# Optimization experiments

Measured on AMD Instinct MI355X. Metric: run time of the kernel, lower is better.

## Reference

```python
import jax, jax.numpy as jnp
import numpy as np

# bitsandbytes FP4 code table (magnitudes), signed -> 16 codes (two zeros, harmless)
_FP4_MAGS = np.array([0.0, 0.0052083333, 1.0/6.0, 0.25, 1.0/3.0, 0.5, 2.0/3.0, 1.0], dtype=np.float32)
_FP4_CODES = np.sort(np.concatenate([-_FP4_MAGS, _FP4_MAGS])).astype(np.float32)
_FP4_BOUNDS = ((_FP4_CODES[:-1] + _FP4_CODES[1:]) * 0.5).astype(np.float32)
_BLOCK = 64  # bnb default FP4 blocksize


def fp4_roundtrip(w):
    """Simulate bnb quantize_fp4 -> dequantize_fp4 (blockwise absmax + nearest FP4 code)."""
    shp = w.shape
    wf = w.reshape(-1, _BLOCK)                              # [n_blocks, 64]
    absmax = jnp.max(jnp.abs(wf), axis=1, keepdims=True)    # per-block scale
    n = wf / jnp.maximum(absmax, 1e-12)                     # normalized to [-1, 1]
    idx = jnp.searchsorted(jnp.asarray(_FP4_BOUNDS), n)     # nearest-code index
    deq = jnp.asarray(_FP4_CODES)[idx] * absmax             # dequantized values
    return deq.reshape(shp)


def setup_inputs() -> dict:
    key = jax.random.key(0)
    k1, k2 = jax.random.split(key)
    in_features, out_features, tokens = 4096, 11008, 8192
    x = jax.random.normal(k1, (tokens, in_features), dtype=jnp.float32)
    weight = jax.random.normal(k2, (out_features, in_features), dtype=jnp.float32) * 0.1
    bias = jnp.zeros((out_features,), dtype=jnp.float32)
    return {"x": x, "weight": weight, "bias": bias}


def reference(x, weight, bias):
    # forward path with quantized weights: dequantize FP4 then matmul + bias
    w = fp4_roundtrip(weight)                # [out, in]
    return jnp.matmul(x, w.T) + bias         # [tokens, out]
```

## Files before the change

kernel.cpp:

```cpp
#include <hip/hip_runtime.h>
#include <hip/hip_bf16.h>
#include <stdint.h>

#define M_DIM 8192
#define N_DIM 11008
#define K_DIM 4096
#define NQB 44032
#define NCB 16384

typedef __attribute__((ext_vector_type(8))) short bf16x8;
typedef __attribute__((ext_vector_type(4))) float f32x4;

__device__ const float kCodes[16] = {
    -1.0f, -(float)(2.0 / 3.0), -0.5f, -(float)(1.0 / 3.0), -0.25f,
    -(float)(1.0 / 6.0), -0.0052083333f, -0.0f,
    0.0f, 0.0052083333f, (float)(1.0 / 6.0), 0.25f,
    (float)(1.0 / 3.0), 0.5f, (float)(2.0 / 3.0), 1.0f};

__device__ __forceinline__ float fp4_bound(int i) {
  return (kCodes[i] + kCodes[i + 1]) * 0.5f;
}

__device__ __forceinline__ unsigned short f2bf(float f) {
  uint32_t u = __float_as_uint(f);
  u = (u + 0x7FFFu + ((u >> 16) & 1u)) >> 16;
  return (unsigned short)u;
}

__device__ __forceinline__ float fp4_rt(float w, float d, float am) {
  float n = w / d;
  int idx = 0;
#pragma unroll
  for (int i = 0; i < 15; ++i) idx += (n > fp4_bound(i)) ? 1 : 0;
  return kCodes[idx] * am;
}

__device__ __forceinline__ uint32_t pack2(float lo, float hi) {
  return (uint32_t)f2bf(lo) | ((uint32_t)f2bf(hi) << 16);
}

__global__ void prep_kernel(const float* __restrict__ W,
                            unsigned short* __restrict__ Wq,
                            const float* __restrict__ X,
                            uint32_t* __restrict__ Y) {
  const int bid = blockIdx.x;
  if (bid < NQB) {
    int t = bid * 256 + threadIdx.x;
    size_t base = (size_t)t * 4;
    float4 v = *reinterpret_cast<const float4*>(W + base);
    float am =
        fmaxf(fmaxf(fabsf(v.x), fabsf(v.y)), fmaxf(fabsf(v.z), fabsf(v.w)));
    am = fmaxf(am, __shfl_xor(am, 1));
    am = fmaxf(am, __shfl_xor(am, 2));
    am = fmaxf(am, __shfl_xor(am, 4));
    am = fmaxf(am, __shfl_xor(am, 8));
    float d = fmaxf(am, 1e-12f);
    ushort4 o;
    o.x = f2bf(fp4_rt(v.x, d, am));
    o.y = f2bf(fp4_rt(v.y, d, am));
    o.z = f2bf(fp4_rt(v.z, d, am));
    o.w = f2bf(fp4_rt(v.w, d, am));
    *reinterpret_cast<ushort4*>(Wq + base) = o;
  } else {
    int t = (bid - NQB) * 256 + threadIdx.x;
    size_t base = (size_t)t * 8;
    float4 a = *reinterpret_cast<const float4*>(X + base);
    float4 b = *reinterpret_cast<const float4*>(X + base + 4);
    uint4 o;
    o.x = pack2(a.x, a.y);
    o.y = pack2(a.z, a.w);
    o.z = pack2(b.x, b.y);
    o.w = pack2(b.z, b.w);
    *reinterpret_cast<uint4*>(Y + (size_t)t * 4) = o;
  }
}

#define GLOAD(src, dst)                                                        \
  __builtin_amdgcn_global_load_lds(                                           \
      (const __attribute__((address_space(1))) void*)(src),                   \
      (__attribute__((address_space(3))) void*)(dst), 16, 0, 0)

#define WAIT_LGKM(N)                                                           \
  asm volatile("s_waitcnt lgkmcnt(" #N ")" ::: "memory");                      \
  __builtin_amdgcn_sched_barrier(0);                                           \
  __builtin_amdgcn_s_setprio(1);

#define ENDBAR()                                                               \
  __builtin_amdgcn_s_setprio(0);                                               \
  __builtin_amdgcn_sched_barrier(0);                                           \
  __builtin_amdgcn_s_barrier();

#define ENDBAR_VM0()                                                           \
  __builtin_amdgcn_s_setprio(0);                                               \
  __builtin_amdgcn_sched_barrier(0);                                           \
  asm volatile("s_waitcnt vmcnt(0)" ::: "memory");                             \
  __builtin_amdgcn_s_barrier();

__global__ __launch_bounds__(512, 2) void gemm256_kernel(
    const short* __restrict__ A, const short* __restrict__ B,
    const float* __restrict__ bias, float* __restrict__ C) {
  __shared__ short lds[2][4][8192];

  const int tid = threadIdx.x;
  const int wave = tid >> 6;
  const int lane = tid & 63;
  const int l15 = lane & 15;
  const int q4 = lane >> 4;
  const int wm = wave >> 2;
  const int wn = wave & 3;

  const int bid = blockIdx.x;
  const int g = bid & 7;
  const int idx = bid >> 3;
  const int brow = (g * 4 + (idx & 3)) * 256;
  const int bcol = (idx >> 2) * 256;

  const int srow = tid >> 3;
  const int scol = ((tid & 7) ^ ((tid >> 3) & 7)) << 3;
  const short* Asrc = A + (size_t)(brow + srow) * K_DIM + scol;
  const short* Bsrc = B + (size_t)(bcol + srow) * K_DIM + scol;
  const int wu0 = wave * 512;
  const int wu1 = 4096 + wave * 512;

  auto stageA = [&](int buf, int half, int t) {
    const short* s = Asrc + (size_t)half * 128 * K_DIM + t * 64;
    GLOAD(s, &lds[buf][half][wu0]);
    GLOAD(s + (size_t)64 * K_DIM, &lds[buf][half][wu1]);
  };
  auto stageB = [&](int buf, int half, int t) {
    const short* s = Bsrc + (size_t)half * 128 * K_DIM + t * 64;
    GLOAD(s, &lds[buf][2 + half][wu0]);
    GLOAD(s + (size_t)64 * K_DIM, &lds[buf][2 + half][wu1]);
  };

  const int offk0 = ((q4 ^ (l15 & 7)) << 4);
  const int offk1 = offk0 ^ 64;
  const char* aP[2] = {(const char*)&lds[0][wm][0] + l15 * 128,
                       (const char*)&lds[1][wm][0] + l15 * 128};
  const char* bP[2] = {
      (const char*)&lds[0][2 + (wn >> 1)][0] + (wn & 1) * 8192 + l15 * 128,
      (const char*)&lds[1][2 + (wn >> 1)][0] + (wn & 1) * 8192 + l15 * 128};

  f32x4 acc[8][4] = {};
  bf16x8 afA[4], afB[4], bfA[4], bfB[4];

  stageB(0, 0, 0);
  stageB(0, 1, 0);
  stageA(0, 0, 0);
  stageA(0, 1, 0);
  stageB(1, 0, 1);
  asm volatile("s_waitcnt vmcnt(2)" ::: "memory");
  __builtin_amdgcn_s_barrier();
#pragma unroll
  for (int m = 0; m < 4; ++m) afA[m] = *(const bf16x8*)(aP[0] + m * 2048 + offk0);
#pragma unroll
  for (int n = 0; n < 4; ++n) bfA[n] = *(const bf16x8*)(bP[0] + n * 2048 + offk0);

  for (int i = 0; i < 32; ++i) {
    const int t1 = 2 * i + 1;
    const int t2 = (2 * i + 2 < 64) ? 2 * i + 2 : 63;
    const int t3 = (2 * i + 3 < 64) ? 2 * i + 3 : 63;

#pragma unroll
    for (int m = 0; m < 4; ++m)
      afB[m] = *(const bf16x8*)(aP[0] + (4 + m) * 2048 + offk0);
    stageB(1, 1, t1);
    WAIT_LGKM(4);
#pragma unroll
    for (int m = 0; m < 4; ++m)
#pragma unroll
      for (int n = 0; n < 4; ++n)
        acc[m][n] = __builtin_amdgcn_mfma_f32_16x16x32_bf16(afA[m], bfA[n],
                                                            acc[m][n], 0, 0, 0);
    ENDBAR();

#pragma unroll
    for (int m = 0; m < 4; ++m)
      afA[m] = *(const bf16x8*)(aP[0] + m * 2048 + offk1);
#pragma unroll
    for (int n = 0; n < 4; ++n)
      bfB[n] = *(const bf16x8*)(bP[0] + n * 2048 + offk1);
    stageA(1, 0, t1);
    stageA(1, 1, t1);
    WAIT_LGKM(8);
#pragma unroll
    for (int m = 0; m < 4; ++m)
#pragma unroll
      for (int n = 0; n < 4; ++n)
        acc[4 + m][n] = __builtin_amdgcn_mfma_f32_16x16x32_bf16(
            afB[m], bfA[n], acc[4 + m][n], 0, 0, 0);
    ENDBAR();

#pragma unroll
    for (int m = 0; m < 4; ++m)
      afB[m] = *(const bf16x8*)(aP[0] + (4 + m) * 2048 + offk1);
    WAIT_LGKM(4);
#pragma unroll
    for (int m = 0; m < 4; ++m)
#pragma unroll
      for (int n = 0; n < 4; ++n)
        acc[m][n] = __builtin_amdgcn_mfma_f32_16x16x32_bf16(afA[m], bfB[n],
                                                            acc[m][n], 0, 0, 0);
    ENDBAR_VM0();

#pragma unroll
    for (int m = 0; m < 4; ++m)
      afA[m] = *(const bf16x8*)(aP[1] + m * 2048 + offk0);
#pragma unroll
    for (int n = 0; n < 4; ++n)
      bfA[n] = *(const bf16x8*)(bP[1] + n * 2048 + offk0);
    stageB(0, 0, t2);
    WAIT_LGKM(8);
#pragma unroll
    for (int m = 0; m < 4; ++m)
#pragma unroll
      for (int n = 0; n < 4; ++n)
        acc[4 + m][n] = __builtin_amdgcn_mfma_f32_16x16x32_bf16(
            afB[m], bfB[n], acc[4 + m][n], 0, 0, 0);
    ENDBAR();

#pragma unroll
    for (int m = 0; m < 4; ++m)
      afB[m] = *(const bf16x8*)(aP[1] + (4 + m) * 2048 + offk0);
    stageB(0, 1, t2);
    WAIT_LGKM(4);
#pragma unroll
    for (int m = 0; m < 4; ++m)
#pragma unroll
      for (int n = 0; n < 4; ++n)
        acc[m][n] = __builtin_amdgcn_mfma_f32_16x16x32_bf16(afA[m], bfA[n],
                                                            acc[m][n], 0, 0, 0);
    ENDBAR();

#pragma unroll
    for (int m = 0; m < 4; ++m)
      afA[m] = *(const bf16x8*)(aP[1] + m * 2048 + offk1);
#pragma unroll
    for (int n = 0; n < 4; ++n)
      bfB[n] = *(const bf16x8*)(bP[1] + n * 2048 + offk1);
    stageA(0, 0, t2);
    stageA(0, 1, t2);
    WAIT_LGKM(8);
#pragma unroll
    for (int m = 0; m < 4; ++m)
#pragma unroll
      for (int n = 0; n < 4; ++n)
        acc[4 + m][n] = __builtin_amdgcn_mfma_f32_16x16x32_bf16(
            afB[m], bfA[n], acc[4 + m][n], 0, 0, 0);
    ENDBAR();

#pragma unroll
    for (int m = 0; m < 4; ++m)
      afB[m] = *(const bf16x8*)(aP[1] + (4 + m) * 2048 + offk1);
    WAIT_LGKM(4);
#pragma unroll
    for (int m = 0; m < 4; ++m)
#pragma unroll
      for (int n = 0; n < 4; ++n)
        acc[m][n] = __builtin_amdgcn_mfma_f32_16x16x32_bf16(afA[m], bfB[n],
                                                            acc[m][n], 0, 0, 0);
    ENDBAR_VM0();

#pragma unroll
    for (int m = 0; m < 4; ++m)
      afA[m] = *(const bf16x8*)(aP[0] + m * 2048 + offk0);
#pragma unroll
    for (int n = 0; n < 4; ++n)
      bfA[n] = *(const bf16x8*)(bP[0] + n * 2048 + offk0);
    stageB(1, 0, t3);
    WAIT_LGKM(8);
#pragma unroll
    for (int m = 0; m < 4; ++m)
#pragma unroll
      for (int n = 0; n < 4; ++n)
        acc[4 + m][n] = __builtin_amdgcn_mfma_f32_16x16x32_bf16(
            afB[m], bfB[n], acc[4 + m][n], 0, 0, 0);
    ENDBAR();
  }

  const int crow0 = brow + wm * 128 + q4 * 4;
  const int ccol0 = bcol + wn * 64 + l15;
#pragma unroll
  for (int n = 0; n < 4; ++n) {
    const float bv = bias[ccol0 + n * 16];
#pragma unroll
    for (int m = 0; m < 8; ++m) {
      const size_t rb = (size_t)(crow0 + m * 16) * N_DIM + (ccol0 + n * 16);
#pragma unroll
      for (int j = 0; j < 4; ++j) C[rb + (size_t)j * N_DIM] = acc[m][n][j] + bv;
    }
  }
}

__global__ __launch_bounds__(256, 2) void gemm_bt_kernel(
    const short* __restrict__ A, const short* __restrict__ B,
    const float* __restrict__ bias, float* __restrict__ C) {
  __shared__ short Alds[128 * 32];
  __shared__ short Blds[128 * 32];

  const int tid = threadIdx.x;
  const int wave = tid >> 6;
  const int lane = tid & 63;
  const int wr = wave >> 1;
  const int wc = wave & 1;

  const int bid = blockIdx.x;
  const int brow = (bid & 63) * 128;
  const int bcol = (80 + (bid >> 6)) * 128;

  const int tr = tid >> 2;
  const int tc = (tid & 3) * 8;
  const short* Ag = A + (size_t)(brow + tr) * K_DIM + tc;
  const short* Bg = B + (size_t)(bcol + tr) * K_DIM + tc;

  short* AldsW = &Alds[wave * 512];
  short* BldsW = &Blds[wave * 512];

  f32x4 acc[4][4] = {};

  const int la = (lane & 15) * 32 + (lane >> 4) * 8;
  const short* Ar = &Alds[(wr * 64) * 32 + la];
  const short* Br = &Blds[(wc * 64) * 32 + la];

  for (int k0 = 0; k0 < K_DIM; k0 += 32) {
    GLOAD(Ag, AldsW);
    GLOAD(Ag + (size_t)64 * K_DIM, AldsW + 2048);
    GLOAD(Bg, BldsW);
    GLOAD(Bg + (size_t)64 * K_DIM, BldsW + 2048);
    __syncthreads();

    bf16x8 af[4], bfr[4];
#pragma unroll
    for (int m = 0; m < 4; ++m)
      af[m] = *reinterpret_cast<const bf16x8*>(Ar + m * 16 * 32);
#pragma unroll
    for (int n = 0; n < 4; ++n)
      bfr[n] = *reinterpret_cast<const bf16x8*>(Br + n * 16 * 32);

#pragma unroll
    for (int m = 0; m < 4; ++m)
#pragma unroll
      for (int n = 0; n < 4; ++n)
        acc[m][n] = __builtin_amdgcn_mfma_f32_16x16x32_bf16(af[m], bfr[n],
                                                            acc[m][n], 0, 0, 0);

    __syncthreads();
    Ag += 32;
    Bg += 32;
  }

  const int crow0 = brow + wr * 64 + (lane >> 4) * 4;
  const int ccol0 = bcol + wc * 64 + (lane & 15);
#pragma unroll
  for (int n = 0; n < 4; ++n) {
    const int cc = ccol0 + n * 16;
    const float bv = bias[cc];
#pragma unroll
    for (int m = 0; m < 4; ++m) {
      const size_t rbase = (size_t)(crow0 + m * 16) * N_DIM + cc;
#pragma unroll
      for (int j = 0; j < 4; ++j) C[rbase + (size_t)j * N_DIM] = acc[m][n][j] + bv;
    }
  }
}

extern "C" void kernel_launch(void* const* d_in, const int* in_sizes, int n_in,
                              void* d_out, int out_size, void* d_ws, size_t ws_size,
                              hipStream_t stream) {
  const float* x = (const float*)d_in[0];
  const float* w = (const float*)d_in[1];
  const float* bias = (const float*)d_in[2];
  float* out = (float*)d_out;

  unsigned short* wq = (unsigned short*)d_ws;
  unsigned short* xb = wq + (size_t)N_DIM * K_DIM;

  prep_kernel<<<NQB + NCB, 256, 0, stream>>>(w, wq, x, (uint32_t*)xb);
  gemm256_kernel<<<dim3(1280), 512, 0, stream>>>((const short*)xb,
                                                 (const short*)wq, bias, out);
  gemm_bt_kernel<<<dim3(384), 256, 0, stream>>>((const short*)xb,
                                                (const short*)wq, bias, out);
}
```

Before: 761.9 us.

## Merge main and edge-tile GEMM kernels into one combined launch

The 256x256 main GEMM kernel and the 128x128 edge-column GEMM kernel become one kernel, dispatched by block index. Blocks at index NMAIN and above run the edge path, with two 256-thread groups per 512-thread block, each using half of the shared LDS buffer. The intent is to let edge tiles fill the idle slots in the partial last wave of main tiles and to remove the serialization between the two launches. The cost is that the edge path now shares the main kernel's 512-thread, large-LDS launch bounds, and its whole-block __syncthreads couples the two groups.

```diff
diff --git a/kernel.cpp b/kernel.cpp
--- a/kernel.cpp
+++ b/kernel.cpp
@@ -7,6 +7,7 @@
 #define K_DIM 4096
 #define NQB 44032
 #define NCB 16384
+#define NMAIN 1280
 
 typedef __attribute__((ext_vector_type(8))) short bf16x8;
 typedef __attribute__((ext_vector_type(4))) float f32x4;
@@ -96,270 +97,273 @@
   asm volatile("s_waitcnt vmcnt(0)" ::: "memory");                             \
   __builtin_amdgcn_s_barrier();
 
-__global__ __launch_bounds__(512, 2) void gemm256_kernel(
+__global__ __launch_bounds__(512, 2) void gemm_comb_kernel(
     const short* __restrict__ A, const short* __restrict__ B,
     const float* __restrict__ bias, float* __restrict__ C) {
   __shared__ short lds[2][4][8192];
 
   const int tid = threadIdx.x;
-  const int wave = tid >> 6;
   const int lane = tid & 63;
-  const int l15 = lane & 15;
-  const int q4 = lane >> 4;
-  const int wm = wave >> 2;
-  const int wn = wave & 3;
-
-  const int bid = blockIdx.x;
-  const int g = bid & 7;
-  const int idx = bid >> 3;
-  const int brow = (g * 4 + (idx & 3)) * 256;
-  const int bcol = (idx >> 2) * 256;
-
-  const int srow = tid >> 3;
-  const int scol = ((tid & 7) ^ ((tid >> 3) & 7)) << 3;
-  const short* Asrc = A + (size_t)(brow + srow) * K_DIM + scol;
-  const short* Bsrc = B + (size_t)(bcol + srow) * K_DIM + scol;
-  const int wu0 = wave * 512;
-  const int wu1 = 4096 + wave * 512;
-
-  auto stageA = [&](int buf, int half, int t) {
-    const short* s = Asrc + (size_t)half * 128 * K_DIM + t * 64;
-    GLOAD(s, &lds[buf][half][wu0]);
-    GLOAD(s + (size_t)64 * K_DIM, &lds[buf][half][wu1]);
-  };
-  auto stageB = [&](int buf, int half, int t) {
-    const short* s = Bsrc + (size_t)half * 128 * K_DIM + t * 64;
-    GLOAD(s, &lds[buf][2 + half][wu0]);
-    GLOAD(s + (size_t)64 * K_DIM, &lds[buf][2 + half][wu1]);
-  };
-
-  const int offk0 = ((q4 ^ (l15 & 7)) << 4);
-  const int offk1 = offk0 ^ 64;
-  const char* aP[2] = {(const char*)&lds[0][wm][0] + l15 * 128,
-                       (const char*)&lds[1][wm][0] + l15 * 128};
-  const char* bP[2] = {
-      (const char*)&lds[0][2 + (wn >> 1)][0] + (wn & 1) * 8192 + l15 * 128,
-      (const char*)&lds[1][2 + (wn >> 1)][0] + (wn & 1) * 8192 + l15 * 128};
-
-  f32x4 acc[8][4] = {};
-  bf16x8 afA[4], afB[4], bfA[4], bfB[4];
-
-  stageB(0, 0, 0);
-  stageB(0, 1, 0);
-  stageA(0, 0, 0);
-  stageA(0, 1, 0);
-  stageB(1, 0, 1);
-  asm volatile("s_waitcnt vmcnt(2)" ::: "memory");
-  __builtin_amdgcn_s_barrier();
-#pragma unroll
-  for (int m = 0; m < 4; ++m) afA[m] = *(const bf16x8*)(aP[0] + m * 2048 + offk0);
-#pragma unroll
-  for (int n = 0; n < 4; ++n) bfA[n] = *(const bf16x8*)(bP[0] + n * 2048 + offk0);
-
-  for (int i = 0; i < 32; ++i) {
-    const int t1 = 2 * i + 1;
-    const int t2 = (2 * i + 2 < 64) ? 2 * i + 2 : 63;
-    const int t3 = (2 * i + 3 < 64) ? 2 * i + 3 : 63;
-
-#pragma unroll
-    for (int m = 0; m < 4; ++m)
-      afB[m] = *(const bf16x8*)(aP[0] + (4 + m) * 2048 + offk0);
-    stageB(1, 1, t1);
-    WAIT_LGKM(4);
-#pragma unroll
-    for (int m = 0; m < 4; ++m)
-#pragma unroll
-      for (int n = 0; n < 4; ++n)
-        acc[m][n] = __builtin_amdgcn_mfma_f32_16x16x32_bf16(afA[m], bfA[n],
-                                                            acc[m][n], 0, 0, 0);
-    ENDBAR();
-
-#pragma unroll
-    for (int m = 0; m < 4; ++m)
-      afA[m] = *(const bf16x8*)(aP[0] + m * 2048 + offk1);
-#pragma unroll
-    for (int n = 0; n < 4; ++n)
-      bfB[n] = *(const bf16x8*)(bP[0] + n * 2048 + offk1);
-    stageA(1, 0, t1);
-    stageA(1, 1, t1);
-    WAIT_LGKM(8);
-#pragma unroll
-    for (int m = 0; m < 4; ++m)
-#pragma unroll
-      for (int n = 0; n < 4; ++n)
-        acc[4 + m][n] = __builtin_amdgcn_mfma_f32_16x16x32_bf16(
-            afB[m], bfA[n], acc[4 + m][n], 0, 0, 0);
-    ENDBAR();
-
-#pragma unroll
-    for (int m = 0; m < 4; ++m)
-      afB[m] = *(const bf16x8*)(aP[0] + (4 + m) * 2048 + offk1);
-    WAIT_LGKM(4);
-#pragma unroll
-    for (int m = 0; m < 4; ++m)
-#pragma unroll
-      for (int n = 0; n < 4; ++n)
-        acc[m][n] = __builtin_amdgcn_mfma_f32_16x16x32_bf16(afA[m], bfB[n],
-                                                            acc[m][n], 0, 0, 0);
-    ENDBAR_VM0();
-
-#pragma unroll
-    for (int m = 0; m < 4; ++m)
-      afA[m] = *(const bf16x8*)(aP[1] + m * 2048 + offk0);
-#pragma unroll
-    for (int n = 0; n < 4; ++n)
-      bfA[n] = *(const bf16x8*)(bP[1] + n * 2048 + offk0);
-    stageB(0, 0, t2);
-    WAIT_LGKM(8);
-#pragma unroll
-    for (int m = 0; m < 4; ++m)
-#pragma unroll
-      for (int n = 0; n < 4; ++n)
-        acc[4 + m][n] = __builtin_amdgcn_mfma_f32_16x16x32_bf16(
-            afB[m], bfB[n], acc[4 + m][n], 0, 0, 0);
-    ENDBAR();
-
-#pragma unroll
-    for (int m = 0; m < 4; ++m)
-      afB[m] = *(const bf16x8*)(aP[1] + (4 + m) * 2048 + offk0);
-    stageB(0, 1, t2);
-    WAIT_LGKM(4);
-#pragma unroll
-    for (int m = 0; m < 4; ++m)
-#pragma unroll
-      for (int n = 0; n < 4; ++n)
-        acc[m][n] = __builtin_amdgcn_mfma_f32_16x16x32_bf16(afA[m], bfA[n],
-                                                            acc[m][n], 0, 0, 0);
-    ENDBAR();
-
-#pragma unroll
-    for (int m = 0; m < 4; ++m)
-      afA[m] = *(const bf16x8*)(aP[1] + m * 2048 + offk1);
-#pragma unroll
-    for (int n = 0; n < 4; ++n)
-      bfB[n] = *(const bf16x8*)(bP[1] + n * 2048 + offk1);
-    stageA(0, 0, t2);
-    stageA(0, 1, t2);
-    WAIT_LGKM(8);
-#pragma unroll
-    for (int m = 0; m < 4; ++m)
-#pragma unroll
-      for (int n = 0; n < 4; ++n)
-        acc[4 + m][n] = __builtin_amdgcn_mfma_f32_16x16x32_bf16(
-            afB[m], bfA[n], acc[4 + m][n], 0, 0, 0);
-    ENDBAR();
-
-#pragma unroll
-    for (int m = 0; m < 4; ++m)
-      afB[m] = *(const bf16x8*)(aP[1] + (4 + m) * 2048 + offk1);
-    WAIT_LGKM(4);
-#pragma unroll
-    for (int m = 0; m < 4; ++m)
-#pragma unroll
-      for (int n = 0; n < 4; ++n)
-        acc[m][n] = __builtin_amdgcn_mfma_f32_16x16x32_bf16(afA[m], bfB[n],
-                                                            acc[m][n], 0, 0, 0);
-    ENDBAR_VM0();
-
+
+  if (blockIdx.x < NMAIN) {
+    const int wave = tid >> 6;
+    const int l15 = lane & 15;
+    const int q4 = lane >> 4;
+    const int wm = wave >> 2;
+    const int wn = wave & 3;
+
+    const int bid = blockIdx.x;
+    const int g = bid & 7;
+    const int idx = bid >> 3;
+    const int brow = (g * 4 + (idx & 3)) * 256;
+    const int bcol = (idx >> 2) * 256;
+
+    const int srow = tid >> 3;
+    const int scol = ((tid & 7) ^ ((tid >> 3) & 7)) << 3;
+    const short* Asrc = A + (size_t)(brow + srow) * K_DIM + scol;
+    const short* Bsrc = B + (size_t)(bcol + srow) * K_DIM + scol;
+    const int wu0 = wave * 512;
+    const int wu1 = 4096 + wave * 512;
+
+    auto stageA = [&](int buf, int half, int t) {
+      const short* s = Asrc + (size_t)half * 128 * K_DIM + t * 64;
+      GLOAD(s, &lds[buf][half][wu0]);
+      GLOAD(s + (size_t)64 * K_DIM, &lds[buf][half][wu1]);
+    };
+    auto stageB = [&](int buf, int half, int t) {
+      const short* s = Bsrc + (size_t)half * 128 * K_DIM + t * 64;
+      GLOAD(s, &lds[buf][2 + half][wu0]);
+      GLOAD(s + (size_t)64 * K_DIM, &lds[buf][2 + half][wu1]);
+    };
+
+    const int offk0 = ((q4 ^ (l15 & 7)) << 4);
+    const int offk1 = offk0 ^ 64;
+    const char* aP[2] = {(const char*)&lds[0][wm][0] + l15 * 128,
+                         (const char*)&lds[1][wm][0] + l15 * 128};
+    const char* bP[2] = {
+        (const char*)&lds[0][2 + (wn >> 1)][0] + (wn & 1) * 8192 + l15 * 128,
+        (const char*)&lds[1][2 + (wn >> 1)][0] + (wn & 1) * 8192 + l15 * 128};
+
+    f32x4 acc[8][4] = {};
+    bf16x8 afA[4], afB[4], bfA[4], bfB[4];
+
+    stageB(0, 0, 0);
+    stageB(0, 1, 0);
+    stageA(0, 0, 0);
+    stageA(0, 1, 0);
+    stageB(1, 0, 1);
+    asm volatile("s_waitcnt vmcnt(2)" ::: "memory");
+    __builtin_amdgcn_s_barrier();
 #pragma unroll
     for (int m = 0; m < 4; ++m)
       afA[m] = *(const bf16x8*)(aP[0] + m * 2048 + offk0);
 #pragma unroll
     for (int n = 0; n < 4; ++n)
       bfA[n] = *(const bf16x8*)(bP[0] + n * 2048 + offk0);
-    stageB(1, 0, t3);
-    WAIT_LGKM(8);
-#pragma unroll
-    for (int m = 0; m < 4; ++m)
-#pragma unroll
-      for (int n = 0; n < 4; ++n)
-        acc[4 + m][n] = __builtin_amdgcn_mfma_f32_16x16x32_bf16(
-            afB[m], bfB[n], acc[4 + m][n], 0, 0, 0);
-    ENDBAR();
-  }
-
-  const int crow0 = brow + wm * 128 + q4 * 4;
-  const int ccol0 = bcol + wn * 64 + l15;
-#pragma unroll
-  for (int n = 0; n < 4; ++n) {
-    const float bv = bias[ccol0 + n * 16];
-#pragma unroll
-    for (int m = 0; m < 8; ++m) {
-      const size_t rb = (size_t)(crow0 + m * 16) * N_DIM + (ccol0 + n * 16);
-#pragma unroll
-      for (int j = 0; j < 4; ++j) C[rb + (size_t)j * N_DIM] = acc[m][n][j] + bv;
+
+    for (int i = 0; i < 32; ++i) {
+      const int t1 = 2 * i + 1;
+      const int t2 = (2 * i + 2 < 64) ? 2 * i + 2 : 63;
+      const int t3 = (2 * i + 3 < 64) ? 2 * i + 3 : 63;
+
+#pragma unroll
+      for (int m = 0; m < 4; ++m)
+        afB[m] = *(const bf16x8*)(aP[0] + (4 + m) * 2048 + offk0);
+      stageB(1, 1, t1);
+      WAIT_LGKM(4);
+#pragma unroll
+      for (int m = 0; m < 4; ++m)
+#pragma unroll
+        for (int n = 0; n < 4; ++n)
+          acc[m][n] = __builtin_amdgcn_mfma_f32_16x16x32_bf16(
+              afA[m], bfA[n], acc[m][n], 0, 0, 0);
+      ENDBAR();
+
+#pragma unroll
+      for (int m = 0; m < 4; ++m)
+        afA[m] = *(const bf16x8*)(aP[0] + m * 2048 + offk1);
+#pragma unroll
+      for (int n = 0; n < 4; ++n)
+        bfB[n] = *(const bf16x8*)(bP[0] + n * 2048 + offk1);
+      stageA(1, 0, t1);
+      stageA(1, 1, t1);
+      WAIT_LGKM(8);
+#pragma unroll
+      for (int m = 0; m < 4; ++m)
+#pragma unroll
+        for (int n = 0; n < 4; ++n)
+          acc[4 + m][n] = __builtin_amdgcn_mfma_f32_16x16x32_bf16(
+              afB[m], bfA[n], acc[4 + m][n], 0, 0, 0);
+      ENDBAR();
+
+#pragma unroll
+      for (int m = 0; m < 4; ++m)
+        afB[m] = *(const bf16x8*)(aP[0] + (4 + m) * 2048 + offk1);
+      WAIT_LGKM(4);
+#pragma unroll
+      for (int m = 0; m < 4; ++m)
+#pragma unroll
+        for (int n = 0; n < 4; ++n)
+          acc[m][n] = __builtin_amdgcn_mfma_f32_16x16x32_bf16(
+              afA[m], bfB[n], acc[m][n], 0, 0, 0);
+      ENDBAR_VM0();
+
+#pragma unroll
+      for (int m = 0; m < 4; ++m)
+        afA[m] = *(const bf16x8*)(aP[1] + m * 2048 + offk0);
+#pragma unroll
+      for (int n = 0; n < 4; ++n)
+        bfA[n] = *(const bf16x8*)(bP[1] + n * 2048 + offk0);
+      stageB(0, 0, t2);
+      WAIT_LGKM(8);
+#pragma unroll
+      for (int m = 0; m < 4; ++m)
+#pragma unroll
+        for (int n = 0; n < 4; ++n)
+          acc[4 + m][n] = __builtin_amdgcn_mfma_f32_16x16x32_bf16(
+              afB[m], bfB[n], acc[4 + m][n], 0, 0, 0);
+      ENDBAR();
+
+#pragma unroll
+      for (int m = 0; m < 4; ++m)
+        afB[m] = *(const bf16x8*)(aP[1] + (4 + m) * 2048 + offk0);
+      stageB(0, 1, t2);
+      WAIT_LGKM(4);
+#pragma unroll
+      for (int m = 0; m < 4; ++m)
+#pragma unroll
+        for (int n = 0; n < 4; ++n)
+          acc[m][n] = __builtin_amdgcn_mfma_f32_16x16x32_bf16(
+              afA[m], bfA[n], acc[m][n], 0, 0, 0);
+      ENDBAR();
+
+#pragma unroll
+      for (int m = 0; m < 4; ++m)
+        afA[m] = *(const bf16x8*)(aP[1] + m * 2048 + offk1);
+#pragma unroll
+      for (int n = 0; n < 4; ++n)
+        bfB[n] = *(const bf16x8*)(bP[1] + n * 2048 + offk1);
+      stageA(0, 0, t2);
+      stageA(0, 1, t2);
+      WAIT_LGKM(8);
+#pragma unroll
+      for (int m = 0; m < 4; ++m)
+#pragma unroll
+        for (int n = 0; n < 4; ++n)
+          acc[4 + m][n] = __builtin_amdgcn_mfma_f32_16x16x32_bf16(
+              afB[m], bfA[n], acc[4 + m][n], 0, 0, 0);
+      ENDBAR();
+
+#pragma unroll
+      for (int m = 0; m < 4; ++m)
+        afB[m] = *(const bf16x8*)(aP[1] + (4 + m) * 2048 + offk1);
+      WAIT_LGKM(4);
+#pragma unroll
+      for (int m = 0; m < 4; ++m)
+#pragma unroll
+        for (int n = 0; n < 4; ++n)
+          acc[m][n] = __builtin_amdgcn_mfma_f32_16x16x32_bf16(
+              afA[m], bfB[n], acc[m][n], 0, 0, 0);
+      ENDBAR_VM0();
+
+#pragma unroll
+      for (int m = 0; m < 4; ++m)
+        afA[m] = *(const bf16x8*)(aP[0] + m * 2048 + offk0);
+#pragma unroll
+      for (int n = 0; n < 4; ++n)
+        bfA[n] = *(const bf16x8*)(bP[0] + n * 2048 + offk0);
+      stageB(1, 0, t3);
+      WAIT_LGKM(8);
+#pragma unroll
+      for (int m = 0; m < 4; ++m)
+#pragma unroll
+        for (int n = 0; n < 4; ++n)
+          acc[4 + m][n] = __builtin_amdgcn_mfma_f32_16x16x32_bf16(
+              afB[m], bfB[n], acc[4 + m][n], 0, 0, 0);
+      ENDBAR();
     }
-  }
-}
-
-__global__ __launch_bounds__(256, 2) void gemm_bt_kernel(
-    const short* __restrict__ A, const short* __restrict__ B,
-    const float* __restrict__ bias, float* __restrict__ C) {
-  __shared__ short Alds[128 * 32];
-  __shared__ short Blds[128 * 32];
-
-  const int tid = threadIdx.x;
-  const int wave = tid >> 6;
-  const int lane = tid & 63;
-  const int wr = wave >> 1;
-  const int wc = wave & 1;
-
-  const int bid = blockIdx.x;
-  const int brow = (bid & 63) * 128;
-  const int bcol = (80 + (bid >> 6)) * 128;
-
-  const int tr = tid >> 2;
-  const int tc = (tid & 3) * 8;
-  const short* Ag = A + (size_t)(brow + tr) * K_DIM + tc;
-  const short* Bg = B + (size_t)(bcol + tr) * K_DIM + tc;
-
-  short* AldsW = &Alds[wave * 512];
-  short* BldsW = &Blds[wave * 512];
-
-  f32x4 acc[4][4] = {};
-
-  const int la = (lane & 15) * 32 + (lane >> 4) * 8;
-  const short* Ar = &Alds[(wr * 64) * 32 + la];
-  const short* Br = &Blds[(wc * 64) * 32 + la];
-
-  for (int k0 = 0; k0 < K_DIM; k0 += 32) {
-    GLOAD(Ag, AldsW);
-    GLOAD(Ag + (size_t)64 * K_DIM, AldsW + 2048);
-    GLOAD(Bg, BldsW);
-    GLOAD(Bg + (size_t)64 * K_DIM, BldsW + 2048);
-    __syncthreads();
-
-    bf16x8 af[4], bfr[4];
-#pragma unroll
-    for (int m = 0; m < 4; ++m)
-      af[m] = *reinterpret_cast<const bf16x8*>(Ar + m * 16 * 32);
-#pragma unroll
-    for (int n = 0; n < 4; ++n)
-      bfr[n] = *reinterpret_cast<const bf16x8*>(Br + n * 16 * 32);
-
-#pragma unroll
-    for (int m = 0; m < 4; ++m)
-#pragma unroll
-      for (int n = 0; n < 4; ++n)
-        acc[m][n] = __builtin_amdgcn_mfma_f32_16x16x32_bf16(af[m], bfr[n],
-                                                            acc[m][n], 0, 0, 0);
-
-    __syncthreads();
-    Ag += 32;
-    Bg += 32;
-  }
-
-  const int crow0 = brow + wr * 64 + (lane >> 4) * 4;
-  const int ccol0 = bcol + wc * 64 + (lane & 15);
-#pragma unroll
-  for (int n = 0; n < 4; ++n) {
-    const int cc = ccol0 + n * 16;
-    const float bv = bias[cc];
-#pragma unroll
-    for (int m = 0; m < 4; ++m) {
-      const size_t rbase = (size_t)(crow0 + m * 16) * N_DIM + cc;
-#pragma unroll
-      for (int j = 0; j < 4; ++j) C[rbase + (size_t)j * N_DIM] = acc[m][n][j] + bv;
+
+    const int crow0 = brow + wm * 128 + q4 * 4;
+    const int ccol0 = bcol + wn * 64 + l15;
+#pragma unroll
+    for (int n = 0; n < 4; ++n) {
+      const float bv = bias[ccol0 + n * 16];
+#pragma unroll
+      for (int m = 0; m < 8; ++m) {
+        const size_t rb = (size_t)(crow0 + m * 16) * N_DIM + (ccol0 + n * 16);
+#pragma unroll
+        for (int j = 0; j < 4; ++j)
+          C[rb + (size_t)j * N_DIM] = acc[m][n][j] + bv;
+      }
+    }
+  } else {
+    const int grp = tid >> 8;
+    const int tg = tid & 255;
+    const int w4 = tg >> 6;
+    const int wr = w4 >> 1;
+    const int wc = w4 & 1;
+
+    const int t = (blockIdx.x - NMAIN) * 2 + grp;
+    const int brow = (t & 63) * 128;
+    const int bcol = (80 + (t >> 6)) * 128;
+
+    short* Alds = &lds[grp][0][0];
+    short* Blds = &lds[grp][1][0];
+
+    const int tr = tg >> 2;
+    const int tc = (tg & 3) * 8;
+    const short* Ag = A + (size_t)(brow + tr) * K_DIM + tc;
+    const short* Bg = B + (size_t)(bcol + tr) * K_DIM + tc;
+
+    short* AldsW = Alds + w4 * 512;
+    short* BldsW = Blds + w4 * 512;
+
+    f32x4 acc[4][4] = {};
+
+    const int la = (lane & 15) * 32 + (lane >> 4) * 8;
+    const short* Ar = Alds + (wr * 64) * 32 + la;
+    const short* Br = Blds + (wc * 64) * 32 + la;
+
+    for (int k0 = 0; k0 < K_DIM; k0 += 32) {
+      GLOAD(Ag, AldsW);
+      GLOAD(Ag + (size_t)64 * K_DIM, AldsW + 2048);
+      GLOAD(Bg, BldsW);
+      GLOAD(Bg + (size_t)64 * K_DIM, BldsW + 2048);
+      __syncthreads();
+
+      bf16x8 af[4], bfr[4];
+#pragma unroll
+      for (int m = 0; m < 4; ++m)
+        af[m] = *reinterpret_cast<const bf16x8*>(Ar + m * 16 * 32);
+#pragma unroll
+      for (int n = 0; n < 4; ++n)
+        bfr[n] = *reinterpret_cast<const bf16x8*>(Br + n * 16 * 32);
+
+#pragma unroll
+      for (int m = 0; m < 4; ++m)
+#pragma unroll
+        for (int n = 0; n < 4; ++n)
+          acc[m][n] = __builtin_amdgcn_mfma_f32_16x16x32_bf16(
+              af[m], bfr[n], acc[m][n], 0, 0, 0);
+
+      __syncthreads();
+      Ag += 32;
+      Bg += 32;
+    }
+
+    const int crow0 = brow + wr * 64 + (lane >> 4) * 4;
+    const int ccol0 = bcol + wc * 64 + (lane & 15);
+#pragma unroll
+    for (int n = 0; n < 4; ++n) {
+      const int cc = ccol0 + n * 16;
+      const float bv = bias[cc];
+#pragma unroll
+      for (int m = 0; m < 4; ++m) {
+        const size_t rbase = (size_t)(crow0 + m * 16) * N_DIM + cc;
+#pragma unroll
+        for (int j = 0; j < 4; ++j)
+          C[rbase + (size_t)j * N_DIM] = acc[m][n][j] + bv;
+      }
     }
   }
 }
@@ -376,8 +380,6 @@
   unsigned short* xb = wq + (size_t)N_DIM * K_DIM;
 
   prep_kernel<<<NQB + NCB, 256, 0, stream>>>(w, wq, x, (uint32_t*)xb);
-  gemm256_kernel<<<dim3(1280), 512, 0, stream>>>((const short*)xb,
-                                                 (const short*)wq, bias, out);
-  gemm_bt_kernel<<<dim3(384), 256, 0, stream>>>((const short*)xb,
-                                                (const short*)wq, bias, out);
-}
+  gemm_comb_kernel<<<dim3(NMAIN + 192), 512, 0, stream>>>(
+      (const short*)xb, (const short*)wq, bias, out);
+}
```

After: 764.2 us. Within noise of the previous version (+0.3%).
